# Kernel optimization log

Hardware: AMD Instinct MI355X
Metric: run time of the kernel (lower is better)

## Reference

```python
import jax, jax.numpy as jnp
import numpy as np

INTER, COMMAND, MOTOR = 128, 64, 32
UNITS = MOTOR + COMMAND + INTER  # neuron order: motor, command, inter
SENSORY = 64
SENSORY_FANOUT, INTER_FANOUT = 16, 16
REC_CMD_SYN, MOTOR_FANIN = 128, 16
OUTPUT_LEN = 32
ODE_UNFOLDS = 6
EPS = 1e-8


def _build_wiring(rng):
    adj = np.zeros((UNITS, UNITS), np.float32)      # [pre, post]
    sadj = np.zeros((SENSORY, UNITS), np.float32)   # [sensory, post]
    motor = np.arange(0, MOTOR)
    command = np.arange(MOTOR, MOTOR + COMMAND)
    inter = np.arange(MOTOR + COMMAND, UNITS)
    pol = lambda: rng.choice(np.asarray([-1.0, 1.0], np.float32))
    for s in range(SENSORY):
        for d in rng.choice(inter, size=SENSORY_FANOUT, replace=False):
            sadj[s, d] = pol()
    for i in inter:
        for d in rng.choice(command, size=INTER_FANOUT, replace=False):
            adj[i, d] = pol()
    for _ in range(REC_CMD_SYN):
        adj[rng.choice(command), rng.choice(command)] = pol()
    for m in motor:
        for s in rng.choice(command, size=MOTOR_FANIN, replace=False):
            adj[s, m] = pol()
    return adj, sadj


def setup_inputs() -> dict:
    rng = np.random.default_rng(0)
    adj, sadj = _build_wiring(rng)
    u = lambda lo, hi, shp: jnp.asarray(rng.uniform(lo, hi, shp), jnp.float32)
    inp = {
        'inputs': jnp.asarray(rng.standard_normal((32, 32, SENSORY)), jnp.float32),
        'input_w': jnp.ones((SENSORY,), jnp.float32),
        'input_b': jnp.zeros((SENSORY,), jnp.float32),
        'sensory_mu': u(0.3, 0.8, (SENSORY, UNITS)),
        'sensory_sigma': u(3.0, 8.0, (SENSORY, UNITS)),
        'sensory_w': u(0.001, 1.0, (SENSORY, UNITS)),
        'sensory_erev': jnp.asarray(sadj),
        'sensory_mask': jnp.asarray(np.abs(sadj)),
        'mu': u(0.3, 0.8, (UNITS, UNITS)),
        'sigma': u(3.0, 8.0, (UNITS, UNITS)),
        'w': u(0.001, 1.0, (UNITS, UNITS)),
        'erev': jnp.asarray(adj),
        'mask': jnp.asarray(np.abs(adj)),
        'gleak': u(0.001, 1.0, (UNITS,)),
        'vleak': u(-0.2, 0.2, (UNITS,)),
        'cm': u(0.4, 0.6, (UNITS,)),
        'output_w': jnp.ones((MOTOR,), jnp.float32),
        'output_b': jnp.zeros((MOTOR,), jnp.float32),
        'dense_w': jnp.asarray(rng.standard_normal((MOTOR, OUTPUT_LEN)) / np.sqrt(MOTOR), jnp.float32),
        'dense_b': jnp.zeros((OUTPUT_LEN,), jnp.float32),
    }
    return inp


def reference(inputs, input_w, input_b, sensory_mu, sensory_sigma, sensory_w,
              sensory_erev, sensory_mask, mu, sigma, w, erev, mask,
              gleak, vleak, cm, output_w, output_b, dense_w, dense_b):
    # affine input mapping (per sensory feature)
    x = inputs * input_w + input_b  # [B,T,S]
    cm_t = cm * ODE_UNFOLDS        # cm / (elapsed_time / unfolds), elapsed_time=1

    def step(v, xt):  # v: [B,U], xt: [B,S]
        s_act = sensory_w * jax.nn.sigmoid(sensory_sigma * (xt[:, :, None] - sensory_mu)) * sensory_mask  # [B,S,U]
        w_num_s = jnp.sum(s_act * sensory_erev, axis=1)  # [B,U]
        w_den_s = jnp.sum(s_act, axis=1)
        for _ in range(ODE_UNFOLDS):
            w_act = w * jax.nn.sigmoid(sigma * (v[:, :, None] - mu)) * mask  # [B,U,U]
            num = cm_t * v + gleak * vleak + jnp.sum(w_act * erev, axis=1) + w_num_s
            den = cm_t + gleak + jnp.sum(w_act, axis=1) + w_den_s
            v = num / (den + EPS)
        return v, v

    v0 = jnp.zeros((x.shape[0], UNITS), x.dtype)
    _, vs = jax.lax.scan(step, v0, jnp.moveaxis(x, 1, 0))  # [T,B,U]
    motor = vs[..., :MOTOR] * output_w + output_b          # [T,B,M]
    out = jnp.einsum('tbm,mo->bto', motor, dense_w) + dense_b  # [B,T,OUT]
    return out
```

## Files before the change

kernel.cpp:

```cpp
#include <hip/hip_runtime.h>


#define U_N 224
#define S_N 64
#define T_N 32
#define M_N 32
#define C_N 64
#define I_N 128
#define O_N 32
#define NUF 6
#define TJT (T_N * NUF)
#define SEG 48
#define ELLS 24
#define ELLC 64
#define CCK 12
#define KS2 12
#define KI2 8
#define EPSV 1e-8f
#define L2E  1.44269504088896340736f

#define OFF_S2I   0
#define OFF_I2C   12288
#define OFF_CC    28672
#define OFF_M2T   31744
#define OFF_CNT   33792
#define OFF_CONST 34112
#define OFF_DYN   34816

#if __has_builtin(__builtin_amdgcn_rcpf)
#define RCPF(x) __builtin_amdgcn_rcpf(x)
#else
#define RCPF(x) (1.0f / (x))
#endif
#if __has_builtin(__builtin_amdgcn_exp2f)
#define EXP2F(x) __builtin_amdgcn_exp2f(x)
#else
#define EXP2F(x) exp2f(x)
#endif

__device__ __forceinline__ float bfu(unsigned short b) {
    return __uint_as_float(((unsigned int)b) << 16);
}
template <bool BF>
__device__ __forceinline__ float ld(const void* p, int i) {
    if (BF) return bfu(((const unsigned short*)p)[i]);
    return ((const float*)p)[i];
}
__device__ __forceinline__ unsigned short f2bf(float f) {
    unsigned int u = __float_as_uint(f);
    u += 0x7FFFu + ((u >> 16) & 1u);
    return (unsigned short)(u >> 16);
}
template <bool BF>
__device__ __forceinline__ void st_out(void* p, int i, float v) {
    if (BF) ((unsigned short*)p)[i] = f2bf(v);
    else    ((float*)p)[i] = v;
}
__device__ __forceinline__ float sigm2(float t) {
    return RCPF(1.0f + EXP2F(t));
}

template <bool BF>
__device__ void build_body(float* ws,
    const void* g_smu, const void* g_ssig, const void* g_sw,
    const void* g_serev, const void* g_smask,
    const void* g_mu, const void* g_sig, const void* g_w,
    const void* g_erev, const void* g_mask,
    const void* g_gleak, const void* g_vleak, const void* g_cm)
{
    const int tid = threadIdx.x;
    const int gt = blockIdx.x * 256 + tid;
    const int stride = gridDim.x * 256;
    int* cnt = (int*)(ws + OFF_CNT);
    if (gt < U_N) {
        float g = ld<BF>(g_gleak, gt);
        float cmt = ld<BF>(g_cm, gt) * (float)NUF;
        ws[OFF_CONST + gt] = cmt;
        ws[OFF_CONST + U_N + gt] = g * ld<BF>(g_vleak, gt);
        ws[OFF_CONST + 2 * U_N + gt] = cmt + g + EPSV;
    }
    float4* ws4 = (float4*)ws;
    for (int idx = gt; idx < U_N * U_N; idx += stride) {
        if (ld<BF>(g_mask, idx) != 0.f) {
            int pre = idx / U_N, post = idx - pre * U_N;
            float sg = ld<BF>(g_sig, idx) * L2E;
            float smu = sg * ld<BF>(g_mu, idx);
            float we = ld<BF>(g_w, idx) * ld<BF>(g_erev, idx);
            if (post < M_N) {
                int s = atomicAdd(&cnt[256 + post], 1);
                if (s < 16) ws4[OFF_M2T / 4 + s * M_N + post] =
                    make_float4(sg, smu, we, __int_as_float(pre - M_N));
            } else if (post < M_N + C_N) {
                int c = post - M_N;
                if (pre >= M_N + C_N) {
                    int s = atomicAdd(&cnt[128 + c], 1);
                    if (s < ELLC) ws4[OFF_I2C / 4 + c * ELLC + s] =
                        make_float4(sg, smu, we, __int_as_float(pre - M_N - C_N));
                } else {
                    int s = atomicAdd(&cnt[192 + c], 1);
                    if (s < CCK) ws4[OFF_CC / 4 + c * CCK + s] =
                        make_float4(sg, smu, we, __int_as_float(pre - M_N));
                }
            }
        }
    }
    for (int idx = gt; idx < S_N * U_N; idx += stride) {
        if (ld<BF>(g_smask, idx) != 0.f) {
            int pre = idx / U_N;
            int i = (idx - pre * U_N) - (M_N + C_N);
            if (i >= 0) {
                int s = atomicAdd(&cnt[i], 1);
                if (s < ELLS) {
                    float sg = ld<BF>(g_ssig, idx) * L2E;
                    ws4[OFF_S2I / 4 + i * ELLS + s] = make_float4(
                        sg, sg * ld<BF>(g_smu, idx),
                        ld<BF>(g_sw, idx) * ld<BF>(g_serev, idx),
                        __int_as_float(pre));
                }
            }
        }
    }
}

__global__ __launch_bounds__(256) void k_build(
    const void* sniff, const void* g_smu, const void* g_ssig, const void* g_sw,
    const void* g_serev, const void* g_smask, const void* g_mu,
    const void* g_sig, const void* g_w, const void* g_erev, const void* g_mask,
    const void* g_gleak, const void* g_vleak, const void* g_cm, float* ws)
{
    unsigned w0 = *(const unsigned int*)sniff;
    if (w0 == 0x3F800000u)
        build_body<false>(ws, g_smu, g_ssig, g_sw, g_serev, g_smask, g_mu,
                          g_sig, g_w, g_erev, g_mask, g_gleak, g_vleak, g_cm);
    else
        build_body<true>(ws, g_smu, g_ssig, g_sw, g_serev, g_smask, g_mu,
                         g_sig, g_w, g_erev, g_mask, g_gleak, g_vleak, g_cm);
}

template <bool BF>
__device__ void inter_body(float (&xs)[T_N][S_N], float* ws,
                           const void* g_inputs, const void* g_in_w,
                           const void* g_in_b)
{
    const int tid = threadIdx.x, b = blockIdx.x;
    for (int g = tid; g < T_N * S_N; g += 256) {
        int t = g >> 6, s = g & 63;
        xs[t][s] = ld<BF>(g_inputs, (b * T_N + t) * S_N + s) *
                       ld<BF>(g_in_w, s) + ld<BF>(g_in_b, s);
    }
    const int iOwn = tid >> 1, lane2 = tid & 1;
    const float4* ws4 = (const float4*)ws;
    int n = ((const int*)(ws + OFF_CNT))[iOwn];
    float pSg[KS2], pMu[KS2], pW[KS2], pWa[KS2]; int pPre[KS2];
    #pragma unroll
    for (int k = 0; k < KS2; ++k) {
        int s = lane2 + (k << 1);
        if (s < n) {
            float4 q = ws4[OFF_S2I / 4 + iOwn * ELLS + s];
            pSg[k] = q.x; pMu[k] = q.y; pW[k] = q.z; pPre[k] = __float_as_int(q.w);
        } else { pSg[k] = 0.f; pMu[k] = 0.f; pW[k] = 0.f; pPre[k] = 0; }
        pWa[k] = fabsf(pW[k]);
    }
    const float cmtI = ws[OFF_CONST + M_N + C_N + iOwn];
    const float baseI = ws[OFF_CONST + U_N + M_N + C_N + iOwn];
    const float cgeI = ws[OFF_CONST + 2 * U_N + M_N + C_N + iOwn];
    __syncthreads();
    float* wVI = ws + OFF_DYN + (size_t)b * TJT * I_N;
    float vi = 0.f;
    for (int t = 0; t < T_N; ++t) {
        float vv[KS2];
        #pragma unroll
        for (int k = 0; k < KS2; ++k) vv[k] = xs[t][pPre[k]];
        float accS = 0.f, accD = 0.f;
        #pragma unroll
        for (int k = 0; k < KS2; ++k) {
            float sg = sigm2(fmaf(-pSg[k], vv[k], pMu[k]));
            accS = fmaf(pW[k], sg, accS);
            accD = fmaf(pWa[k], sg, accD);
        }
        accS += __shfl_xor(accS, 1, 2);
        accD += __shfl_xor(accD, 1, 2);
        float rden = RCPF(cgeI + accD);
        float A = cmtI * rden, Bv = (baseI + accS) * rden;
        #pragma unroll
        for (int j = 0; j < NUF; ++j) {
            if (lane2 == 0) wVI[(t * NUF + j) * I_N + iOwn] = vi;
            vi = fmaf(A, vi, Bv);
        }
    }
}

__global__ __launch_bounds__(256) void k_inter(
    const void* sniff, const void* g_inputs, const void* g_in_w,
    const void* g_in_b, float* ws)
{
    __shared__ float xs[T_N][S_N];
    unsigned w0 = *(const unsigned int*)sniff;
    if (w0 == 0x3F800000u) inter_body<false>(xs, ws, g_inputs, g_in_w, g_in_b);
    else                   inter_body<true>(xs, ws, g_inputs, g_in_w, g_in_b);
}

__global__ __launch_bounds__(512) void k_i2c(float* ws)
{
    __shared__ float  vi_s[8 * I_N];
    __shared__ float2 scs[8 * C_N];
    const int tid = threadIdx.x, b = blockIdx.x, tj0 = blockIdx.y * 8;
    const int B = gridDim.x;
    const float* wVI = ws + OFF_DYN + ((size_t)b * TJT + tj0) * I_N;
    float2* wSC = (float2*)(ws + OFF_DYN + (size_t)B * TJT * I_N) +
                  ((size_t)b * TJT + tj0) * C_N;
    for (int g = tid; g < 8 * I_N; g += 512) vi_s[g] = wVI[g];
    const int cOwn = tid >> 3, lane8 = tid & 7;
    int n = ((const int*)(ws + OFF_CNT))[128 + cOwn];
    const float4* ws4 = (const float4*)ws;
    float pSg[KI2], pMu[KI2], pW[KI2], pWa[KI2]; int pPre[KI2];
    #pragma unroll
    for (int k = 0; k < KI2; ++k) {
        int s = lane8 + (k << 3);
        if (s < n) {
            float4 q = ws4[OFF_I2C / 4 + cOwn * ELLC + s];
            pSg[k] = q.x; pMu[k] = q.y; pW[k] = q.z; pPre[k] = __float_as_int(q.w);
        } else { pSg[k] = 0.f; pMu[k] = 0.f; pW[k] = 0.f; pPre[k] = 0; }
        pWa[k] = fabsf(pW[k]);
    }
    __syncthreads();
    for (int r = 0; r < 8; ++r) {
        const float* row = vi_s + r * I_N;
        float vv[KI2];
        #pragma unroll
        for (int k = 0; k < KI2; ++k) vv[k] = row[pPre[k]];
        float accS = 0.f, accD = 0.f;
        #pragma unroll
        for (int k = 0; k < KI2; ++k) {
            float sg = sigm2(fmaf(-pSg[k], vv[k], pMu[k]));
            accS = fmaf(pW[k], sg, accS);
            accD = fmaf(pWa[k], sg, accD);
        }
        accS += __shfl_xor(accS, 1, 8);
        accS += __shfl_xor(accS, 2, 8);
        accS += __shfl_xor(accS, 4, 8);
        accD += __shfl_xor(accD, 1, 8);
        accD += __shfl_xor(accD, 2, 8);
        accD += __shfl_xor(accD, 4, 8);
        if (lane8 == 0) scs[r * C_N + cOwn] = make_float2(accS, accD);
    }
    __syncthreads();
    wSC[tid] = scs[tid];
}

struct SmemC {
    float ct[TJT][C_N];
    union {
        float2 sb[2][SEG][C_N];
        float2 mAB[TJT][M_N];
    } u;
    float moutS[T_N][M_N];
    float dwS[M_N * O_N];
};

template <bool BF>
__device__ void cmdmo_body(SmemC& s, float* ws, const void* g_ow,
                           const void* g_ob, const void* g_dw,
                           const void* g_db, void* __restrict__ g_out)
{
    const int tid = threadIdx.x, b = blockIdx.x, B = gridDim.x;
    const float2* wSC = (const float2*)(ws + OFF_DYN + (size_t)B * TJT * I_N) +
                        (size_t)b * TJT * C_N;
    for (int g = tid; g < M_N * O_N; g += 256) s.dwS[g] = ld<BF>(g_dw, g);
    for (int g = tid; g < SEG * C_N; g += 256)
        (&s.u.sb[0][0][0])[g] = wSC[g];

    float pSg[CCK], pMu[CCK], pW[CCK], pWa[CCK]; int pPre[CCK];
    float cmtC = 0.f, baseC = 0.f, cgeC = 0.f;
    if (tid < C_N) {
        int n = ((const int*)(ws + OFF_CNT))[192 + tid];
        const float4* ws4 = (const float4*)ws;
        #pragma unroll
        for (int k = 0; k < CCK; ++k) {
            if (k < n) {
                float4 q = ws4[OFF_CC / 4 + tid * CCK + k];
                pSg[k] = q.x; pMu[k] = q.y; pW[k] = q.z;
                pPre[k] = __float_as_int(q.w);
            } else { pSg[k] = 0.f; pMu[k] = 0.f; pW[k] = 0.f; pPre[k] = 0; }
            pWa[k] = fabsf(pW[k]);
        }
        cmtC = ws[OFF_CONST + M_N + tid];
        baseC = ws[OFF_CONST + U_N + M_N + tid];
        cgeC = ws[OFF_CONST + 2 * U_N + M_N + tid];
    }
    __syncthreads();

    float vC = 0.f;
    for (int seg = 0; seg < 4; ++seg) {
        if (tid < C_N) {
            const int lane = tid;
            const float2* scb = &s.u.sb[seg & 1][0][0];
            for (int r = 0; r < SEG; ++r) {
                const int tj = seg * SEG + r;
                s.ct[tj][lane] = vC;
                float vv[CCK];
                #pragma unroll
                for (int kk = 0; kk < CCK; ++kk)
                    vv[kk] = s.ct[tj][pPre[kk]];
                float2 sd = scb[r * C_N + lane];
                float accS = 0.f, accD = 0.f;
                #pragma unroll
                for (int kk = 0; kk < CCK; ++kk) {
                    float sg = sigm2(fmaf(-pSg[kk], vv[kk], pMu[kk]));
                    accS = fmaf(pW[kk], sg, accS);
                    accD = fmaf(pWa[kk], sg, accD);
                }
                vC = fmaf(cmtC, vC, baseC + sd.x + accS) *
                     RCPF(cgeC + sd.y + accD);
            }
        } else if (seg < 3) {
            float2* dst = &s.u.sb[(seg + 1) & 1][0][0];
            const float2* src = wSC + (size_t)(seg + 1) * SEG * C_N;
            for (int g = tid - 64; g < SEG * C_N; g += 192) dst[g] = src[g];
        }
        __syncthreads();
    }

    const int m = tid & 31;
    const float4* ws4 = (const float4*)ws;
    float4 q[16];
    #pragma unroll
    for (int k = 0; k < 16; ++k) q[k] = ws4[OFF_M2T / 4 + k * M_N + m];
    const float cmtM = ws[OFF_CONST + m];
    const float baseM = ws[OFF_CONST + U_N + m];
    const float cgeM = ws[OFF_CONST + 2 * U_N + m];
    for (int g = tid; g < TJT * M_N; g += 256) {
        int tj = g >> 5;
        const float* crow = s.ct[tj];
        float vv[16];
        #pragma unroll
        for (int k = 0; k < 16; ++k) vv[k] = crow[__float_as_int(q[k].w)];
        float accS = 0.f, accD = 0.f;
        #pragma unroll
        for (int k = 0; k < 16; ++k) {
            float sg = sigm2(fmaf(-q[k].x, vv[k], q[k].y));
            float wv = q[k].z * sg;
            accS += wv; accD += fabsf(wv);
        }
        float rden = RCPF(cgeM + accD);
        s.u.mAB[tj][m] = make_float2(cmtM * rden, (baseM + accS) * rden);
    }
    __syncthreads();

    if (tid < M_N) {
        float ow = ld<BF>(g_ow, tid), ob = ld<BF>(g_ob, tid);
        float vM = 0.f;
        for (int t = 0; t < T_N; ++t) {
            #pragma unroll
            for (int j = 0; j < NUF; ++j) {
                float2 ab = s.u.mAB[t * NUF + j][tid];
                vM = fmaf(ab.x, vM, ab.y);
            }
            s.moutS[t][tid] = fmaf(vM, ow, ob);
        }
    }
    __syncthreads();

    for (int g = tid; g < T_N * O_N; g += 256) {
        int t = g >> 5, o = g & 31;
        float acc = ld<BF>(g_db, o);
        #pragma unroll 8
        for (int mm = 0; mm < M_N; ++mm)
            acc += s.moutS[t][mm] * s.dwS[mm * O_N + o];
        st_out<BF>(g_out, (b * T_N + t) * O_N + o, acc);
    }
}

__global__ __launch_bounds__(256) void k_cmdmo(
    const void* sniff, float* ws, const void* g_ow, const void* g_ob,
    const void* g_dw, const void* g_db, void* __restrict__ g_out)
{
    __shared__ SmemC s;
    unsigned w0 = *(const unsigned int*)sniff;
    if (w0 == 0x3F800000u) cmdmo_body<false>(s, ws, g_ow, g_ob, g_dw, g_db, g_out);
    else                   cmdmo_body<true>(s, ws, g_ow, g_ob, g_dw, g_db, g_out);
}

#define MONO_NT 640
#define CH  4
#define NCH (T_N / CH)
#define TJ  (CH * NUF)
#define KI  8
#define KS  6

struct SmemM {
    float cmt[U_N], base[U_N], cge[U_N];
    float4 m2t[16][M_N];
    float mout[T_N][M_N];
    union {
        struct {
            unsigned short ell_c[C_N][ELLC];
            unsigned short ell_s[I_N][ELLS];
            float4 cc[C_N][CCK];
            int cnt_c[C_N], cnt_s[I_N], cnt_cc[C_N], cnt_m[M_N];
        } b;
        struct {
            float  x[CH][S_N];
            float  Vi[TJ][I_N];
            float2 sc[2][TJ][C_N];
            float  ctraj[TJ][C_N];
            float2 mAB[TJ][M_N];
        } r;
    } u;
};

template <bool BF>
__device__ void mono_body(SmemM& sm,
    const void* g_inputs, const void* g_in_w, const void* g_in_b,
    const void* g_smu, const void* g_ssig, const void* g_sw,
    const void* g_serev, const void* g_smask,
    const void* g_mu, const void* g_sig, const void* g_w,
    const void* g_erev, const void* g_mask,
    const void* g_gleak, const void* g_vleak, const void* g_cm,
    const void* g_ow, const void* g_ob, const void* g_dw, const void* g_db,
    void* __restrict__ g_out)
{
    const int tid = threadIdx.x;
    const int b = blockIdx.x;
    const int p = tid - 64;
    const bool wp = (p >= 0 && p < 512);
    const bool isMo = (p >= 512 && p < 512 + M_N);

    if (tid < U_N) {
        float g = ld<BF>(g_gleak, tid);
        float cmt = ld<BF>(g_cm, tid) * (float)NUF;
        sm.cmt[tid] = cmt;
        sm.base[tid] = g * ld<BF>(g_vleak, tid);
        sm.cge[tid] = cmt + g + EPSV;
    }
    if (tid < C_N) { sm.u.b.cnt_c[tid] = 0; sm.u.b.cnt_cc[tid] = 0; }
    if (tid < I_N) sm.u.b.cnt_s[tid] = 0;
    if (tid < M_N) sm.u.b.cnt_m[tid] = 0;
    if (tid < 512) sm.m2t[tid >> 5][tid & 31] =
        make_float4(0.f, 0.f, 0.f, __int_as_float(0));
    __syncthreads();

    for (int idx = tid; idx < U_N * U_N; idx += MONO_NT) {
        if (ld<BF>(g_mask, idx) != 0.f) {
            int pre = idx / U_N;
            int post = idx - pre * U_N;
            if (post < M_N) {
                int s = atomicAdd(&sm.u.b.cnt_m[post], 1);
                if (s < 16) {
                    float sg = ld<BF>(g_sig, idx) * L2E;
                    float we = ld<BF>(g_w, idx) * ld<BF>(g_erev, idx);
                    sm.m2t[s][post] = make_float4(sg, sg * ld<BF>(g_mu, idx),
                                                  we, __int_as_float(pre - M_N));
                }
            } else if (post < M_N + C_N) {
                int c = post - M_N;
                if (pre >= M_N + C_N) {
                    int s = atomicAdd(&sm.u.b.cnt_c[c], 1);
                    if (s < ELLC) sm.u.b.ell_c[c][s] = (unsigned short)idx;
                } else {
                    int s = atomicAdd(&sm.u.b.cnt_cc[c], 1);
                    if (s < CCK) {
                        float sg = ld<BF>(g_sig, idx) * L2E;
                        float we = ld<BF>(g_w, idx) * ld<BF>(g_erev, idx);
                        sm.u.b.cc[c][s] = make_float4(sg, sg * ld<BF>(g_mu, idx),
                                                      we, __int_as_float(pre - M_N));
                    }
                }
            }
        }
    }
    for (int idx = tid; idx < S_N * U_N; idx += MONO_NT) {
        if (ld<BF>(g_smask, idx) != 0.f) {
            int pre = idx / U_N;
            int i = (idx - pre * U_N) - (M_N + C_N);
            if (i >= 0) {
                int s = atomicAdd(&sm.u.b.cnt_s[i], 1);
                if (s < ELLS) sm.u.b.ell_s[i][s] = (unsigned short)idx;
            }
        }
    }
    __syncthreads();

    const int cOwn = wp ? (p >> 3) : 0, lane8 = wp ? (p & 7) : 0;
    const int iOwn = wp ? (p >> 2) : 0, lane4 = wp ? (p & 3) : 0;
    float iSg[KI], iMu[KI], iW[KI]; int iPre[KI]; int kWi = 0;
    {
        int n = wp ? min(sm.u.b.cnt_c[cOwn], ELLC) : 0;
        #pragma unroll
        for (int k = 0; k < KI; ++k) {
            int s = lane8 + (k << 3);
            iSg[k] = 0.f; iMu[k] = 0.f; iW[k] = 0.f; iPre[k] = 0;
            if (s < n) {
                int flat = sm.u.b.ell_c[cOwn][s];
                float sg = ld<BF>(g_sig, flat) * L2E;
                iSg[k] = sg; iMu[k] = sg * ld<BF>(g_mu, flat);
                iW[k] = ld<BF>(g_w, flat) * ld<BF>(g_erev, flat);
                iPre[k] = flat / U_N - (M_N + C_N);
            }
        }
        kWi = (n + 7) >> 3;
    }
    float sSg[KS], sMu[KS], sW[KS]; int sPre[KS]; int kWs = 0;
    {
        int n = wp ? min(sm.u.b.cnt_s[iOwn], ELLS) : 0;
        #pragma unroll
        for (int k = 0; k < KS; ++k) {
            int s = lane4 + (k << 2);
            sSg[k] = 0.f; sMu[k] = 0.f; sW[k] = 0.f; sPre[k] = 0;
            if (s < n) {
                int flat = sm.u.b.ell_s[iOwn][s];
                float sg = ld<BF>(g_ssig, flat) * L2E;
                sSg[k] = sg; sMu[k] = sg * ld<BF>(g_smu, flat);
                sW[k] = ld<BF>(g_sw, flat) * ld<BF>(g_serev, flat);
                sPre[k] = flat / U_N;
            }
        }
        kWs = (n + 3) >> 2;
    }
    #pragma unroll
    for (int off = 1; off < 64; off <<= 1) {
        int o = __shfl_xor(kWi, off, 64); kWi = (o > kWi) ? o : kWi;
        int q2 = __shfl_xor(kWs, off, 64); kWs = (q2 > kWs) ? q2 : kWs;
    }
    kWi = __builtin_amdgcn_readfirstlane(kWi);
    kWs = __builtin_amdgcn_readfirstlane(kWs);

    float kSg[CCK], kMu[CCK], kW[CCK]; int kPre[CCK]; int ccK = 0;
    float cmtC = 0.f, baseC = 0.f, cgeC = 0.f;
    if (tid < C_N) {
        int n = min(sm.u.b.cnt_cc[tid], CCK);
        #pragma unroll
        for (int k = 0; k < CCK; ++k) {
            if (k < n) {
                float4 q3 = sm.u.b.cc[tid][k];
                kSg[k] = q3.x; kMu[k] = q3.y; kW[k] = q3.z;
                kPre[k] = __float_as_int(q3.w);
            } else { kSg[k] = 0.f; kMu[k] = 0.f; kW[k] = 0.f; kPre[k] = 0; }
        }
        ccK = n;
        #pragma unroll
        for (int off = 1; off < 64; off <<= 1) {
            int o = __shfl_xor(ccK, off, 64);
            ccK = (o > ccK) ? o : ccK;
        }
        ccK = __builtin_amdgcn_readfirstlane(ccK);
        cmtC = sm.cmt[M_N + tid]; baseC = sm.base[M_N + tid];
        cgeC = sm.cge[M_N + tid];
    }
    const float cmtI = sm.cmt[M_N + C_N + iOwn];
    const float baseI = sm.base[M_N + C_N + iOwn];
    const float cgeI = sm.cge[M_N + C_N + iOwn];
    float owR = 0.f, obR = 0.f;
    if (isMo) { owR = ld<BF>(g_ow, p - 512); obR = ld<BF>(g_ob, p - 512); }
    __syncthreads();

    if (wp && p < CH * S_N) {
        int tt = p >> 6, s = p & 63;
        sm.u.r.x[tt][s] = ld<BF>(g_inputs, (b * T_N + tt) * S_N + s) *
                              ld<BF>(g_in_w, s) + ld<BF>(g_in_b, s);
    }
    __syncthreads();

    float vInt = 0.f;
    float vCmd = 0.f;
    float vMot = 0.f;

    for (int i = 0; i <= NCH; ++i) {
        if (tid < C_N) {
            if (i >= 1) {
                const float2* scb = &sm.u.r.sc[(i - 1) & 1][0][0];
                for (int tj = 0; tj < TJ / 2; ++tj) {
                    sm.u.r.ctraj[tj][tid] = vCmd;
                    float accS = 0.f, accD = 0.f;
                    #pragma unroll
                    for (int k = 0; k < CCK; ++k) {
                        if (k < ccK) {
                            float vv = __shfl(vCmd, kPre[k], 64);
                            float sg = sigm2(fmaf(-kSg[k], vv, kMu[k]));
                            float wv = kW[k] * sg;
                            accS += wv; accD += fabsf(wv);
                        }
                    }
                    float2 sd = scb[tj * C_N + tid];
                    vCmd = fmaf(cmtC, vCmd, baseC + sd.x + accS) *
                           RCPF(cgeC + sd.y + accD);
                }
            }
        } else if (wp) {
            if (i < NCH) {
                float vi = vInt;
                for (int tt = 0; tt < CH; ++tt) {
                    float accS = 0.f, accD = 0.f;
                    #pragma unroll
                    for (int k = 0; k < KS; ++k) {
                        if (k < kWs) {
                            float xv = sm.u.r.x[tt][sPre[k]];
                            float sg = sigm2(fmaf(-sSg[k], xv, sMu[k]));
                            float wv = sW[k] * sg;
                            accS += wv; accD += fabsf(wv);
                        }
                    }
                    accS += __shfl_xor(accS, 1, 4); accS += __shfl_xor(accS, 2, 4);
                    accD += __shfl_xor(accD, 1, 4); accD += __shfl_xor(accD, 2, 4);
                    float rden = RCPF(cgeI + accD);
                    float A = cmtI * rden;
                    float Bv = (baseI + accS) * rden;
                    #pragma unroll
                    for (int j = 0; j < NUF; ++j) {
                        if (lane4 == 0) sm.u.r.Vi[tt * NUF + j][iOwn] = vi;
                        vi = fmaf(A, vi, Bv);
                    }
                }
                vInt = vi;
            }
        } else if (isMo && i >= 2) {
            int m = p - 512, c = i - 2;
            for (int tt = 0; tt < CH; ++tt) {
                #pragma unroll
                for (int j = 0; j < NUF; ++j) {
                    float2 ab = sm.u.r.mAB[tt * NUF + j][m];
                    vMot = fmaf(ab.x, vMot, ab.y);
                }
                sm.mout[c * CH + tt][m] = fmaf(vMot, owR, obR);
            }
        }
        __syncthreads();

        if (tid < C_N) {
            if (i >= 1) {
                const float2* scb = &sm.u.r.sc[(i - 1) & 1][0][0];
                for (int tj = TJ / 2; tj < TJ; ++tj) {
                    sm.u.r.ctraj[tj][tid] = vCmd;
                    float accS = 0.f, accD = 0.f;
                    #pragma unroll
                    for (int k = 0; k < CCK; ++k) {
                        if (k < ccK) {
                            float vv = __shfl(vCmd, kPre[k], 64);
                            float sg = sigm2(fmaf(-kSg[k], vv, kMu[k]));
                            float wv = kW[k] * sg;
                            accS += wv; accD += fabsf(wv);
                        }
                    }
                    float2 sd = scb[tj * C_N + tid];
                    vCmd = fmaf(cmtC, vCmd, baseC + sd.x + accS) *
                           RCPF(cgeC + sd.y + accD);
                }
            }
        } else if (wp) {
            if (i < NCH) {
                float2* scw = &sm.u.r.sc[i & 1][0][0];
                for (int tj = 0; tj < TJ; ++tj) {
                    const float* vrow = &sm.u.r.Vi[tj][0];
                    float accS = 0.f, accD = 0.f;
                    #pragma unroll
                    for (int k = 0; k < KI; ++k) {
                        if (k < kWi) {
                            float vv = vrow[iPre[k]];
                            float sg = sigm2(fmaf(-iSg[k], vv, iMu[k]));
                            float wv = iW[k] * sg;
                            accS += wv; accD += fabsf(wv);
                        }
                    }
                    accS += __shfl_xor(accS, 1, 8);
                    accS += __shfl_xor(accS, 2, 8);
                    accS += __shfl_xor(accS, 4, 8);
                    accD += __shfl_xor(accD, 1, 8);
                    accD += __shfl_xor(accD, 2, 8);
                    accD += __shfl_xor(accD, 4, 8);
                    if (lane8 == 0) scw[tj * C_N + cOwn] = make_float2(accS, accD);
                }
            }
            if (i + 1 < NCH && p < CH * S_N) {
                int tt = p >> 6, s = p & 63;
                sm.u.r.x[tt][s] =
                    ld<BF>(g_inputs, (b * T_N + (i + 1) * CH + tt) * S_N + s) *
                        ld<BF>(g_in_w, s) + ld<BF>(g_in_b, s);
            }
        }
        __syncthreads();

        if (i >= 1) {
            for (int g = tid; g < TJ * M_N; g += MONO_NT) {
                int tj = g >> 5, m = g & 31;
                const float* crow = &sm.u.r.ctraj[tj][0];
                float accS = 0.f, accD = 0.f;
                #pragma unroll
                for (int k = 0; k < 16; ++k) {
                    float4 q4 = sm.m2t[k][m];
                    float vv = crow[__float_as_int(q4.w)];
                    float sg = sigm2(fmaf(-q4.x, vv, q4.y));
                    float wv = q4.z * sg;
                    accS += wv; accD += fabsf(wv);
                }
                float rden = RCPF(sm.cge[m] + accD);
                sm.u.r.mAB[tj][m] = make_float2(sm.cmt[m] * rden,
                                                (sm.base[m] + accS) * rden);
            }
        }
        __syncthreads();
    }

    if (isMo) {
        int m = p - 512, c = NCH - 1;
        for (int tt = 0; tt < CH; ++tt) {
            #pragma unroll
            for (int j = 0; j < NUF; ++j) {
                float2 ab = sm.u.r.mAB[tt * NUF + j][m];
                vMot = fmaf(ab.x, vMot, ab.y);
            }
            sm.mout[c * CH + tt][m] = fmaf(vMot, owR, obR);
        }
    }
    __syncthreads();

    for (int g = tid; g < T_N * O_N; g += MONO_NT) {
        int t = g >> 5, o = g & 31;
        float acc = ld<BF>(g_db, o);
        #pragma unroll 8
        for (int m = 0; m < M_N; ++m)
            acc += sm.mout[t][m] * ld<BF>(g_dw, m * O_N + o);
        st_out<BF>(g_out, (b * T_N + t) * O_N + o, acc);
    }
}

__global__ __launch_bounds__(MONO_NT) void ncp_mono(
    const void* i0,  const void* i1,  const void* i2,  const void* i3,
    const void* i4,  const void* i5,  const void* i6,  const void* i7,
    const void* i8,  const void* i9,  const void* i10, const void* i11,
    const void* i12, const void* i13, const void* i14, const void* i15,
    const void* i16, const void* i17, const void* i18, const void* i19,
    void* __restrict__ g_out)
{
    __shared__ SmemM sm;
    unsigned w0 = *(const unsigned int*)i1;
    if (w0 == 0x3F800000u)
        mono_body<false>(sm, i0, i1, i2, i3, i4, i5, i6, i7, i8, i9, i10, i11,
                         i12, i13, i14, i15, i16, i17, i18, i19, g_out);
    else
        mono_body<true>(sm, i0, i1, i2, i3, i4, i5, i6, i7, i8, i9, i10, i11,
                        i12, i13, i14, i15, i16, i17, i18, i19, g_out);
}

extern "C" void kernel_launch(void* const* d_in, const int* in_sizes, int n_in,
                              void* d_out, int out_size, void* d_ws, size_t ws_size,
                              hipStream_t stream) {
    (void)n_in; (void)out_size;
    const int B = in_sizes[0] / (T_N * S_N);
    float* ws = (float*)d_ws;
    const size_t req = ((size_t)OFF_DYN + (size_t)B * TJT * I_N +
                        (size_t)B * TJT * C_N * 2) * sizeof(float);
    if (d_ws != nullptr && ws_size >= req) {
        hipMemsetAsync((char*)d_ws + (size_t)OFF_CNT * sizeof(float), 0,
                       288 * sizeof(int), stream);
        k_build<<<dim3(32), dim3(256), 0, stream>>>(
            d_in[1], d_in[3], d_in[4], d_in[5], d_in[6], d_in[7], d_in[8],
            d_in[9], d_in[10], d_in[11], d_in[12], d_in[13], d_in[14],
            d_in[15], ws);
        k_inter<<<dim3(B), dim3(256), 0, stream>>>(
            d_in[1], d_in[0], d_in[1], d_in[2], ws);
        k_i2c<<<dim3(B, TJT / 8), dim3(512), 0, stream>>>(ws);
        k_cmdmo<<<dim3(B), dim3(256), 0, stream>>>(
            d_in[1], ws, d_in[16], d_in[17], d_in[18], d_in[19], d_out);
    } else {
        ncp_mono<<<dim3(B), dim3(MONO_NT), 0, stream>>>(
            d_in[0],  d_in[1],  d_in[2],  d_in[3],  d_in[4],  d_in[5],
            d_in[6],  d_in[7],  d_in[8],  d_in[9],  d_in[10], d_in[11],
            d_in[12], d_in[13], d_in[14], d_in[15], d_in[16], d_in[17],
            d_in[18], d_in[19], d_out);
    }
}
```

Measured before the change: 199.3 us.

## Use wavefront shuffles and register prefetch in command-neuron recurrence

The sequential command-neuron recurrence now reads neighbour voltages with cross-lane shuffles within a single 64-lane wavefront instead of going through shared memory. The double-buffered shared staging, with its helper threads and per-segment barriers, is replaced by a 16-deep register prefetch ring that pulls each step's sensory/inter contributions straight from global memory. The workspace per batch is padded by PFD rows so the prefetch can safely overrun the end, and the fused abs(W) fma becomes multiply plus abs. The aim is to cut LDS latency and synchronisation on the serial critical path, at the cost of more registers and global-load latency that the prefetch depth must hide.

```diff
diff --git a/kernel.cpp b/kernel.cpp
--- a/kernel.cpp
+++ b/kernel.cpp
@@ -10,12 +10,12 @@
 #define O_N 32
 #define NUF 6
 #define TJT (T_N * NUF)
-#define SEG 48
 #define ELLS 24
 #define ELLC 64
 #define CCK 12
 #define KS2 12
 #define KI2 8
+#define PFD 16
 #define EPSV 1e-8f
 #define L2E  1.44269504088896340736f
 
@@ -208,7 +208,7 @@
     const int B = gridDim.x;
     const float* wVI = ws + OFF_DYN + ((size_t)b * TJT + tj0) * I_N;
     float2* wSC = (float2*)(ws + OFF_DYN + (size_t)B * TJT * I_N) +
-                  ((size_t)b * TJT + tj0) * C_N;
+                  ((size_t)b * (TJT + PFD) + tj0) * C_N;
     for (int g = tid; g < 8 * I_N; g += 512) vi_s[g] = wVI[g];
     const int cOwn = tid >> 3, lane8 = tid & 7;
     int n = ((const int*)(ws + OFF_CNT))[128 + cOwn];
@@ -250,10 +250,7 @@
 
 struct SmemC {
     float ct[TJT][C_N];
-    union {
-        float2 sb[2][SEG][C_N];
-        float2 mAB[TJT][M_N];
-    } u;
+    float2 mAB[TJT][M_N];
     float moutS[T_N][M_N];
     float dwS[M_N * O_N];
 };
@@ -264,62 +261,54 @@
                            const void* g_db, void* __restrict__ g_out)
 {
     const int tid = threadIdx.x, b = blockIdx.x, B = gridDim.x;
-    const float2* wSC = (const float2*)(ws + OFF_DYN + (size_t)B * TJT * I_N) +
-                        (size_t)b * TJT * C_N;
     for (int g = tid; g < M_N * O_N; g += 256) s.dwS[g] = ld<BF>(g_dw, g);
-    for (int g = tid; g < SEG * C_N; g += 256)
-        (&s.u.sb[0][0][0])[g] = wSC[g];
-
-    float pSg[CCK], pMu[CCK], pW[CCK], pWa[CCK]; int pPre[CCK];
-    float cmtC = 0.f, baseC = 0.f, cgeC = 0.f;
+
     if (tid < C_N) {
-        int n = ((const int*)(ws + OFF_CNT))[192 + tid];
+        const int lane = tid;
+        int n = ((const int*)(ws + OFF_CNT))[192 + lane];
         const float4* ws4 = (const float4*)ws;
+        float pSg[CCK], pMu[CCK], pW[CCK]; int pPre[CCK];
         #pragma unroll
         for (int k = 0; k < CCK; ++k) {
             if (k < n) {
-                float4 q = ws4[OFF_CC / 4 + tid * CCK + k];
+                float4 q = ws4[OFF_CC / 4 + lane * CCK + k];
                 pSg[k] = q.x; pMu[k] = q.y; pW[k] = q.z;
                 pPre[k] = __float_as_int(q.w);
             } else { pSg[k] = 0.f; pMu[k] = 0.f; pW[k] = 0.f; pPre[k] = 0; }
-            pWa[k] = fabsf(pW[k]);
-        }
-        cmtC = ws[OFF_CONST + M_N + tid];
-        baseC = ws[OFF_CONST + U_N + M_N + tid];
-        cgeC = ws[OFF_CONST + 2 * U_N + M_N + tid];
-    }
-    __syncthreads();
-
-    float vC = 0.f;
-    for (int seg = 0; seg < 4; ++seg) {
-        if (tid < C_N) {
-            const int lane = tid;
-            const float2* scb = &s.u.sb[seg & 1][0][0];
-            for (int r = 0; r < SEG; ++r) {
-                const int tj = seg * SEG + r;
-                s.ct[tj][lane] = vC;
+        }
+        const float cmtC = ws[OFF_CONST + M_N + lane];
+        const float baseC = ws[OFF_CONST + U_N + M_N + lane];
+        const float cgeC = ws[OFF_CONST + 2 * U_N + M_N + lane];
+        const float2* wSC = (const float2*)(ws + OFF_DYN + (size_t)B * TJT * I_N) +
+                            (size_t)b * (TJT + PFD) * C_N + lane;
+        float2 pf[PFD];
+        #pragma unroll
+        for (int k = 0; k < PFD; ++k) pf[k] = wSC[(size_t)k * C_N];
+        float vC = 0.f;
+        for (int tj0 = 0; tj0 < TJT; tj0 += PFD) {
+            #pragma unroll
+            for (int k = 0; k < PFD; ++k) {
+                const int tj = tj0 + k;
                 float vv[CCK];
                 #pragma unroll
                 for (int kk = 0; kk < CCK; ++kk)
-                    vv[kk] = s.ct[tj][pPre[kk]];
-                float2 sd = scb[r * C_N + lane];
+                    vv[kk] = __shfl(vC, pPre[kk], 64);
+                s.ct[tj][lane] = vC;
+                float2 sd = pf[k];
+                pf[k] = wSC[(size_t)(tj + PFD) * C_N];
                 float accS = 0.f, accD = 0.f;
                 #pragma unroll
                 for (int kk = 0; kk < CCK; ++kk) {
                     float sg = sigm2(fmaf(-pSg[kk], vv[kk], pMu[kk]));
-                    accS = fmaf(pW[kk], sg, accS);
-                    accD = fmaf(pWa[kk], sg, accD);
+                    float wv = pW[kk] * sg;
+                    accS += wv; accD += fabsf(wv);
                 }
                 vC = fmaf(cmtC, vC, baseC + sd.x + accS) *
                      RCPF(cgeC + sd.y + accD);
             }
-        } else if (seg < 3) {
-            float2* dst = &s.u.sb[(seg + 1) & 1][0][0];
-            const float2* src = wSC + (size_t)(seg + 1) * SEG * C_N;
-            for (int g = tid - 64; g < SEG * C_N; g += 192) dst[g] = src[g];
-        }
-        __syncthreads();
-    }
+        }
+    }
+    __syncthreads();
 
     const int m = tid & 31;
     const float4* ws4 = (const float4*)ws;
@@ -343,7 +332,7 @@
             accS += wv; accD += fabsf(wv);
         }
         float rden = RCPF(cgeM + accD);
-        s.u.mAB[tj][m] = make_float2(cmtM * rden, (baseM + accS) * rden);
+        s.mAB[tj][m] = make_float2(cmtM * rden, (baseM + accS) * rden);
     }
     __syncthreads();
 
@@ -353,7 +342,7 @@
         for (int t = 0; t < T_N; ++t) {
             #pragma unroll
             for (int j = 0; j < NUF; ++j) {
-                float2 ab = s.u.mAB[t * NUF + j][tid];
+                float2 ab = s.mAB[t * NUF + j][tid];
                 vM = fmaf(ab.x, vM, ab.y);
             }
             s.moutS[t][tid] = fmaf(vM, ow, ob);
@@ -748,7 +737,7 @@
     const int B = in_sizes[0] / (T_N * S_N);
     float* ws = (float*)d_ws;
     const size_t req = ((size_t)OFF_DYN + (size_t)B * TJT * I_N +
-                        (size_t)B * TJT * C_N * 2) * sizeof(float);
+                        (size_t)B * (TJT + PFD) * C_N * 2) * sizeof(float);
     if (d_ws != nullptr && ws_size >= req) {
         hipMemsetAsync((char*)d_ws + (size_t)OFF_CNT * sizeof(float), 0,
                        288 * sizeof(int), stream);
```

Result: no change. 200.9 us (+0.8%).
